# Kernel optimization log

Measured on AMD Instinct MI355X. Metric: run time of the kernel, lower is better.

Reference implementation:

```python
import jax, jax.numpy as jnp
import numpy as np

DIM = 512
HEADS = 8
WINDOW = 128


def setup_inputs() -> dict:
    key = jax.random.key(0)
    k1, k2, k3, k4 = jax.random.split(key, 4)
    x = jax.random.normal(k1, (16, 4096, DIM), dtype=jnp.float32)
    w_qkv = jax.random.normal(k2, (3 * DIM, DIM), dtype=jnp.float32) * 0.02
    w_proj = jax.random.normal(k3, (DIM, DIM), dtype=jnp.float32) * 0.02
    b_proj = jax.random.normal(k4, (DIM,), dtype=jnp.float32) * 0.02
    return {"x": x, "w_qkv": w_qkv, "w_proj": w_proj, "b_proj": b_proj}


def reference(x, w_qkv, w_proj, b_proj):
    B0, T0, C = x.shape
    H = HEADS
    hd = C // H
    scale = hd ** (-0.5)
    W = WINDOW
    # split into independent windows: [B*T/W, W, C]
    xw = x.reshape(-1, W, C)
    Bw = xw.shape[0]
    # qkv projection (no bias), reshape to [3, Bw, H, W, hd]
    qkv = (xw @ w_qkv.T).reshape(Bw, W, 3, H, hd).transpose(2, 0, 3, 1, 4)
    q, k, v = qkv[0], qkv[1], qkv[2]
    # scaled scores per window: [Bw, H, W, W]
    attn = jnp.einsum("bhqd,bhkd->bhqk", q, k) * scale
    causal_mask = jnp.tril(jnp.ones((W, W), dtype=bool))
    attn = jnp.where(causal_mask, attn, -jnp.inf)
    attn = jax.nn.softmax(attn, axis=-1)
    out = jnp.einsum("bhqk,bhkd->bhqd", attn, v)  # [Bw, H, W, hd]
    out = out.transpose(0, 2, 1, 3).reshape(Bw, W, C)
    out = out @ w_proj.T + b_proj
    return out.reshape(B0, T0, C)
```

## Files before the change

### kernel.cpp

```cpp
#include <hip/hip_runtime.h>
#include <stdint.h>


typedef unsigned short ushort_t;
typedef __attribute__((ext_vector_type(8))) short short8;
typedef __attribute__((ext_vector_type(4))) float f32x4;
typedef __attribute__((ext_vector_type(4))) float f4v;
typedef __attribute__((ext_vector_type(4))) unsigned short us4;

static __device__ __forceinline__ unsigned short f2bf(float f) {
  unsigned int u = __float_as_uint(f);
  u += 0x7FFFu + ((u >> 16) & 1u);
  return (unsigned short)(u >> 16);
}

static __device__ __forceinline__ void gl_lds16(const ushort_t* g, ushort_t* l) {
  __builtin_amdgcn_global_load_lds(
      (const __attribute__((address_space(1))) void*)g,
      (__attribute__((address_space(3))) void*)l, 16, 0, 0);
}

__global__ __launch_bounds__(256) void cast_f32_bf16(const float* __restrict__ in,
                                                     ushort_t* __restrict__ out, int n4) {
  int i = blockIdx.x * 256 + threadIdx.x;
  if (i >= n4) return;
  f4v v = ((const f4v*)in)[i];
  us4 o;
  o.x = f2bf(v.x); o.y = f2bf(v.y); o.z = f2bf(v.z); o.w = f2bf(v.w);
  ((us4*)out)[i] = o;
}

__global__ __launch_bounds__(256) void qkv_gemm(const ushort_t* __restrict__ A,
                                                const ushort_t* __restrict__ B,
                                                ushort_t* __restrict__ qk,
                                                ushort_t* __restrict__ vT) {
  __shared__ __align__(16) ushort_t As[128 * 64];
  __shared__ __align__(16) ushort_t Bs[128 * 64];
  const int tid = threadIdx.x;
  const int lane = tid & 63;
  const int wv = tid >> 6;
  const int wr = wv >> 1, wc = wv & 1;
  const int m0 = blockIdx.y << 7;
  const int n0 = blockIdx.x << 7;
  const int lr = lane & 15;
  const int lg = lane >> 4;
  const int lk = lg << 3;

  f32x4 acc[4][4] = {};

  const int grow = tid >> 3;
  const int gcol = (tid & 7) << 3;
  const ushort_t* gA = A + (size_t)(m0 + grow) * 512 + gcol;
  const ushort_t* gB = B + (size_t)(n0 + grow) * 512 + gcol;

  for (int kk = 0; kk < 512; kk += 64) {
#pragma unroll
    for (int r = 0; r < 4; ++r) {
      gl_lds16(gA + (size_t)(r * 32) * 512 + kk, As + (size_t)(r * 256 + wv * 64) * 8);
      gl_lds16(gB + (size_t)(r * 32) * 512 + kk, Bs + (size_t)(r * 256 + wv * 64) * 8);
    }
    __syncthreads();
#pragma unroll
    for (int ks = 0; ks < 2; ++ks) {
      const int kb = ks * 32 + lk;
      short8 a[4], b[4];
#pragma unroll
      for (int mi = 0; mi < 4; ++mi)
        a[mi] = *(const short8*)(As + (wr * 64 + mi * 16 + lr) * 64 + kb);
#pragma unroll
      for (int ni = 0; ni < 4; ++ni)
        b[ni] = *(const short8*)(Bs + (wc * 64 + ni * 16 + lr) * 64 + kb);
#pragma unroll
      for (int mi = 0; mi < 4; ++mi)
#pragma unroll
        for (int ni = 0; ni < 4; ++ni)
          acc[mi][ni] = __builtin_amdgcn_mfma_f32_16x16x32_bf16(a[mi], b[ni], acc[mi][ni], 0, 0, 0);
    }
    __syncthreads();
  }

  if (n0 < 1024) {
#pragma unroll
    for (int mi = 0; mi < 4; ++mi) {
      const int rbase = m0 + wr * 64 + mi * 16 + lg * 4;
#pragma unroll
      for (int ni = 0; ni < 4; ++ni) {
        const int col = n0 + wc * 64 + ni * 16 + lr;
#pragma unroll
        for (int rg = 0; rg < 4; ++rg)
          qk[(size_t)(rbase + rg) * 1024 + col] = f2bf(acc[mi][ni][rg]);
      }
    }
  } else {
    const int win = blockIdx.y;
#pragma unroll
    for (int mi = 0; mi < 4; ++mi) {
      const int t0 = wr * 64 + mi * 16 + lg * 4;
#pragma unroll
      for (int ni = 0; ni < 4; ++ni) {
        const int c = n0 - 1024 + wc * 64 + ni * 16 + lr;
        const int h = c >> 6, d = c & 63;
        us4 o;
        o.x = f2bf(acc[mi][ni][0]); o.y = f2bf(acc[mi][ni][1]);
        o.z = f2bf(acc[mi][ni][2]); o.w = f2bf(acc[mi][ni][3]);
        *(us4*)(vT + (size_t)((win * 8 + h) * 64 + d) * 128 + t0) = o;
      }
    }
  }
}

__global__ __launch_bounds__(256) void attn_kernel(const ushort_t* __restrict__ qk,
                                                   const ushort_t* __restrict__ vT,
                                                   ushort_t* __restrict__ attn_out) {
  __shared__ __align__(16) ushort_t smem[27136];
  ushort_t* qs = smem;
  ushort_t* ks_ = smem + 9216;
  ushort_t* ps = smem;
  ushort_t* vs = smem + 18432;

  const int tid = threadIdx.x;
  const int lane = tid & 63;
  const int wv = tid >> 6;
  const int win = blockIdx.x >> 3;
  const int h = blockIdx.x & 7;
  const int lr = lane & 15;
  const int lg = lane >> 4;
  const int lk = lg << 3;

  const size_t qbase = (size_t)win * 128 * 1024 + h * 64;
#pragma unroll
  for (int r = 0; r < 4; ++r) {
    const int c = r * 256 + tid;
    const int t = c >> 3, d8 = (c & 7) << 3;
    short8 vq = *(const short8*)(qk + qbase + (size_t)t * 1024 + d8);
    short8 vk = *(const short8*)(qk + qbase + 512 + (size_t)t * 1024 + d8);
    *(short8*)(qs + t * 72 + d8) = vq;
    *(short8*)(ks_ + t * 72 + d8) = vk;
  }
  const size_t vbase = (size_t)(win * 8 + h) * 64 * 128;
#pragma unroll
  for (int r = 0; r < 4; ++r) {
    const int c = r * 256 + tid;
    const int d = c >> 4, t8 = (c & 15) << 3;
    short8 vvv = *(const short8*)(vT + vbase + (size_t)d * 128 + t8);
    *(short8*)(vs + d * 136 + t8) = vvv;
  }
  __syncthreads();

  const int r0 = wv * 32;
  const int ncol = 2 * (wv + 1);
  f32x4 sacc[2][8] = {};
#pragma unroll
  for (int ks2 = 0; ks2 < 2; ++ks2) {
    const int kb = ks2 * 32 + lk;
    short8 a0 = *(const short8*)(qs + (r0 + lr) * 72 + kb);
    short8 a1 = *(const short8*)(qs + (r0 + 16 + lr) * 72 + kb);
#pragma unroll
    for (int ni = 0; ni < 8; ++ni) {
      if (ni < ncol) {
        short8 b = *(const short8*)(ks_ + (ni * 16 + lr) * 72 + kb);
        sacc[0][ni] = __builtin_amdgcn_mfma_f32_16x16x32_bf16(a0, b, sacc[0][ni], 0, 0, 0);
        sacc[1][ni] = __builtin_amdgcn_mfma_f32_16x16x32_bf16(a1, b, sacc[1][ni], 0, 0, 0);
      }
    }
  }

  const float scale = 0.125f;
  float rs[2][4];
#pragma unroll
  for (int mi = 0; mi < 2; ++mi) {
#pragma unroll
    for (int rg = 0; rg < 4; ++rg) {
      const int row = r0 + mi * 16 + lg * 4 + rg;
      float m = -1e30f;
#pragma unroll
      for (int ni = 0; ni < 8; ++ni) {
        if (ni < ncol) {
          const int col = ni * 16 + lr;
          float v = sacc[mi][ni][rg] * scale;
          v = (col <= row) ? v : -1e30f;
          sacc[mi][ni][rg] = v;
          m = fmaxf(m, v);
        }
      }
      m = fmaxf(m, __shfl_xor(m, 1));
      m = fmaxf(m, __shfl_xor(m, 2));
      m = fmaxf(m, __shfl_xor(m, 4));
      m = fmaxf(m, __shfl_xor(m, 8));
      float s = 0.f;
#pragma unroll
      for (int ni = 0; ni < 8; ++ni) {
        if (ni < ncol) {
          float p = __expf(sacc[mi][ni][rg] - m);
          sacc[mi][ni][rg] = p;
          s += p;
        }
      }
      s += __shfl_xor(s, 1);
      s += __shfl_xor(s, 2);
      s += __shfl_xor(s, 4);
      s += __shfl_xor(s, 8);
      rs[mi][rg] = 1.0f / s;
    }
  }

  __syncthreads();

#pragma unroll
  for (int mi = 0; mi < 2; ++mi)
#pragma unroll
    for (int ni = 0; ni < 8; ++ni) {
      if (ni < ncol) {
#pragma unroll
        for (int rg = 0; rg < 4; ++rg) {
          const int row = r0 + mi * 16 + lg * 4 + rg;
          const int col = ni * 16 + lr;
          ps[row * 136 + col] = f2bf(sacc[mi][ni][rg]);
        }
      }
    }

  f32x4 oacc[2][4] = {};
#pragma unroll
  for (int ks2 = 0; ks2 < 4; ++ks2) {
    if (ks2 <= wv) {
      const int kb = ks2 * 32 + lk;
      short8 a0 = *(const short8*)(ps + (r0 + lr) * 136 + kb);
      short8 a1 = *(const short8*)(ps + (r0 + 16 + lr) * 136 + kb);
#pragma unroll
      for (int nd = 0; nd < 4; ++nd) {
        short8 b = *(const short8*)(vs + (nd * 16 + lr) * 136 + kb);
        oacc[0][nd] = __builtin_amdgcn_mfma_f32_16x16x32_bf16(a0, b, oacc[0][nd], 0, 0, 0);
        oacc[1][nd] = __builtin_amdgcn_mfma_f32_16x16x32_bf16(a1, b, oacc[1][nd], 0, 0, 0);
      }
    }
  }

  const size_t obase = (size_t)win * 128 * 512 + h * 64;
#pragma unroll
  for (int mi = 0; mi < 2; ++mi)
#pragma unroll
    for (int nd = 0; nd < 4; ++nd)
#pragma unroll
      for (int rg = 0; rg < 4; ++rg) {
        const int row = r0 + mi * 16 + lg * 4 + rg;
        const int col = nd * 16 + lr;
        attn_out[obase + (size_t)row * 512 + col] = f2bf(oacc[mi][nd][rg] * rs[mi][rg]);
      }
}

__global__ __launch_bounds__(256) void proj_gemm(const ushort_t* __restrict__ A,
                                                 const ushort_t* __restrict__ B,
                                                 const float* __restrict__ bias,
                                                 float* __restrict__ out) {
  __shared__ __align__(16) ushort_t As[128 * 64];
  __shared__ __align__(16) ushort_t Bs[128 * 64];
  const int tid = threadIdx.x;
  const int lane = tid & 63;
  const int wv = tid >> 6;
  const int wr = wv >> 1, wc = wv & 1;
  const int m0 = blockIdx.y << 7;
  const int n0 = blockIdx.x << 7;
  const int lr = lane & 15;
  const int lg = lane >> 4;
  const int lk = lg << 3;

  f32x4 acc[4][4] = {};

  const int grow = tid >> 3;
  const int gcol = (tid & 7) << 3;
  const ushort_t* gA = A + (size_t)(m0 + grow) * 512 + gcol;
  const ushort_t* gB = B + (size_t)(n0 + grow) * 512 + gcol;

  for (int kk = 0; kk < 512; kk += 64) {
#pragma unroll
    for (int r = 0; r < 4; ++r) {
      gl_lds16(gA + (size_t)(r * 32) * 512 + kk, As + (size_t)(r * 256 + wv * 64) * 8);
      gl_lds16(gB + (size_t)(r * 32) * 512 + kk, Bs + (size_t)(r * 256 + wv * 64) * 8);
    }
    __syncthreads();
#pragma unroll
    for (int ks = 0; ks < 2; ++ks) {
      const int kb = ks * 32 + lk;
      short8 a[4], b[4];
#pragma unroll
      for (int mi = 0; mi < 4; ++mi)
        a[mi] = *(const short8*)(As + (wr * 64 + mi * 16 + lr) * 64 + kb);
#pragma unroll
      for (int ni = 0; ni < 4; ++ni)
        b[ni] = *(const short8*)(Bs + (wc * 64 + ni * 16 + lr) * 64 + kb);
#pragma unroll
      for (int mi = 0; mi < 4; ++mi)
#pragma unroll
        for (int ni = 0; ni < 4; ++ni)
          acc[mi][ni] = __builtin_amdgcn_mfma_f32_16x16x32_bf16(a[mi], b[ni], acc[mi][ni], 0, 0, 0);
    }
    __syncthreads();
  }

#pragma unroll
  for (int mi = 0; mi < 4; ++mi) {
    const int rbase = m0 + wr * 64 + mi * 16 + lg * 4;
#pragma unroll
    for (int ni = 0; ni < 4; ++ni) {
      const int col = n0 + wc * 64 + ni * 16 + lr;
      const float bv = bias[col];
#pragma unroll
      for (int rg = 0; rg < 4; ++rg)
        out[(size_t)(rbase + rg) * 512 + col] = acc[mi][ni][rg] + bv;
    }
  }
}

extern "C" void kernel_launch(void* const* d_in, const int* in_sizes, int n_in,
                              void* d_out, int out_size, void* d_ws, size_t ws_size,
                              hipStream_t stream) {
  const float* x      = (const float*)d_in[0];
  const float* w_qkv  = (const float*)d_in[1];
  const float* w_proj = (const float*)d_in[2];
  const float* b_proj = (const float*)d_in[3];
  float* out = (float*)d_out;

  char* ws = (char*)d_ws;
  ushort_t* x_bf     = (ushort_t*)(ws);
  ushort_t* qk_ws    = (ushort_t*)(ws + 67108864);
  ushort_t* vT_ws    = (ushort_t*)(ws + 67108864 + 134217728);
  ushort_t* attn_ws  = (ushort_t*)(ws + 67108864 + 134217728 + 67108864);
  ushort_t* wqkv_bf  = (ushort_t*)(ws + 335544320);
  ushort_t* wproj_bf = (ushort_t*)(ws + 337117184);

  cast_f32_bf16<<<32768, 256, 0, stream>>>(x, x_bf, 8388608);
  cast_f32_bf16<<<768, 256, 0, stream>>>(w_qkv, wqkv_bf, 196608);
  cast_f32_bf16<<<256, 256, 0, stream>>>(w_proj, wproj_bf, 65536);

  qkv_gemm<<<dim3(12, 512), 256, 0, stream>>>(x_bf, wqkv_bf, qk_ws, vT_ws);
  attn_kernel<<<4096, 256, 0, stream>>>(qk_ws, vT_ws, attn_ws);
  proj_gemm<<<dim3(4, 512), 256, 0, stream>>>(attn_ws, wproj_bf, b_proj, out);
}
```

Before: 547.7 us.

## Swizzle GEMM LDS tiles and balance causal attention work across waves

```diff
diff --git a/kernel.cpp b/kernel.cpp
--- a/kernel.cpp
+++ b/kernel.cpp
@@ -44,12 +44,12 @@
   const int n0 = blockIdx.x << 7;
   const int lr = lane & 15;
   const int lg = lane >> 4;
-  const int lk = lg << 3;
+  const int sw = lr & 7;
 
   f32x4 acc[4][4] = {};
 
   const int grow = tid >> 3;
-  const int gcol = (tid & 7) << 3;
+  const int gcol = (((tid & 7) ^ (grow & 7)) << 3);
   const ushort_t* gA = A + (size_t)(m0 + grow) * 512 + gcol;
   const ushort_t* gB = B + (size_t)(n0 + grow) * 512 + gcol;
 
@@ -62,14 +62,14 @@
     __syncthreads();
 #pragma unroll
     for (int ks = 0; ks < 2; ++ks) {
-      const int kb = ks * 32 + lk;
+      const int co = ((((ks << 2) | lg) ^ sw) << 3);
       short8 a[4], b[4];
 #pragma unroll
       for (int mi = 0; mi < 4; ++mi)
-        a[mi] = *(const short8*)(As + (wr * 64 + mi * 16 + lr) * 64 + kb);
+        a[mi] = *(const short8*)(As + (wr * 64 + mi * 16 + lr) * 64 + co);
 #pragma unroll
       for (int ni = 0; ni < 4; ++ni)
-        b[ni] = *(const short8*)(Bs + (wc * 64 + ni * 16 + lr) * 64 + kb);
+        b[ni] = *(const short8*)(Bs + (wc * 64 + ni * 16 + lr) * 64 + co);
 #pragma unroll
       for (int mi = 0; mi < 4; ++mi)
 #pragma unroll
@@ -79,10 +79,11 @@
     __syncthreads();
   }
 
+  const int lg4 = lg << 2;
   if (n0 < 1024) {
 #pragma unroll
     for (int mi = 0; mi < 4; ++mi) {
-      const int rbase = m0 + wr * 64 + mi * 16 + lg * 4;
+      const int rbase = m0 + wr * 64 + mi * 16 + lg4;
 #pragma unroll
       for (int ni = 0; ni < 4; ++ni) {
         const int col = n0 + wc * 64 + ni * 16 + lr;
@@ -95,7 +96,7 @@
     const int win = blockIdx.y;
 #pragma unroll
     for (int mi = 0; mi < 4; ++mi) {
-      const int t0 = wr * 64 + mi * 16 + lg * 4;
+      const int t0 = wr * 64 + mi * 16 + lg4;
 #pragma unroll
       for (int ni = 0; ni < 4; ++ni) {
         const int c = n0 - 1024 + wc * 64 + ni * 16 + lr;
@@ -112,11 +113,11 @@
 __global__ __launch_bounds__(256) void attn_kernel(const ushort_t* __restrict__ qk,
                                                    const ushort_t* __restrict__ vT,
                                                    ushort_t* __restrict__ attn_out) {
-  __shared__ __align__(16) ushort_t smem[27136];
+  __shared__ __align__(16) ushort_t smem[25856];
   ushort_t* qs = smem;
-  ushort_t* ks_ = smem + 9216;
+  ushort_t* ks_ = smem + 8704;
+  ushort_t* vs = smem + 17408;
   ushort_t* ps = smem;
-  ushort_t* vs = smem + 18432;
 
   const int tid = threadIdx.x;
   const int lane = tid & 63;
@@ -126,6 +127,7 @@
   const int lr = lane & 15;
   const int lg = lane >> 4;
   const int lk = lg << 3;
+  const int lg4 = lg << 2;
 
   const size_t qbase = (size_t)win * 128 * 1024 + h * 64;
 #pragma unroll
@@ -134,8 +136,8 @@
     const int t = c >> 3, d8 = (c & 7) << 3;
     short8 vq = *(const short8*)(qk + qbase + (size_t)t * 1024 + d8);
     short8 vk = *(const short8*)(qk + qbase + 512 + (size_t)t * 1024 + d8);
-    *(short8*)(qs + t * 72 + d8) = vq;
-    *(short8*)(ks_ + t * 72 + d8) = vk;
+    *(short8*)(qs + t * 68 + d8) = vq;
+    *(short8*)(ks_ + t * 68 + d8) = vk;
   }
   const size_t vbase = (size_t)(win * 8 + h) * 64 * 128;
 #pragma unroll
@@ -143,23 +145,24 @@
     const int c = r * 256 + tid;
     const int d = c >> 4, t8 = (c & 15) << 3;
     short8 vvv = *(const short8*)(vT + vbase + (size_t)d * 128 + t8);
-    *(short8*)(vs + d * 136 + t8) = vvv;
+    *(short8*)(vs + d * 132 + t8) = vvv;
   }
   __syncthreads();
 
-  const int r0 = wv * 32;
-  const int ncol = 2 * (wv + 1);
+  const int rt[2] = {wv, 7 - wv};
+
   f32x4 sacc[2][8] = {};
 #pragma unroll
   for (int ks2 = 0; ks2 < 2; ++ks2) {
     const int kb = ks2 * 32 + lk;
-    short8 a0 = *(const short8*)(qs + (r0 + lr) * 72 + kb);
-    short8 a1 = *(const short8*)(qs + (r0 + 16 + lr) * 72 + kb);
+    short8 a0 = *(const short8*)(qs + (rt[0] * 16 + lr) * 68 + kb);
+    short8 a1 = *(const short8*)(qs + (rt[1] * 16 + lr) * 68 + kb);
 #pragma unroll
     for (int ni = 0; ni < 8; ++ni) {
-      if (ni < ncol) {
-        short8 b = *(const short8*)(ks_ + (ni * 16 + lr) * 72 + kb);
-        sacc[0][ni] = __builtin_amdgcn_mfma_f32_16x16x32_bf16(a0, b, sacc[0][ni], 0, 0, 0);
+      if (ni <= rt[1]) {
+        short8 b = *(const short8*)(ks_ + (ni * 16 + lr) * 68 + kb);
+        if (ni <= rt[0])
+          sacc[0][ni] = __builtin_amdgcn_mfma_f32_16x16x32_bf16(a0, b, sacc[0][ni], 0, 0, 0);
         sacc[1][ni] = __builtin_amdgcn_mfma_f32_16x16x32_bf16(a1, b, sacc[1][ni], 0, 0, 0);
       }
     }
@@ -169,13 +172,14 @@
   float rs[2][4];
 #pragma unroll
   for (int mi = 0; mi < 2; ++mi) {
+    const int rb = rt[mi] * 16;
 #pragma unroll
     for (int rg = 0; rg < 4; ++rg) {
-      const int row = r0 + mi * 16 + lg * 4 + rg;
+      const int row = rb + lg4 + rg;
       float m = -1e30f;
 #pragma unroll
       for (int ni = 0; ni < 8; ++ni) {
-        if (ni < ncol) {
+        if (ni <= rt[mi]) {
           const int col = ni * 16 + lr;
           float v = sacc[mi][ni][rg] * scale;
           v = (col <= row) ? v : -1e30f;
@@ -190,7 +194,7 @@
       float s = 0.f;
 #pragma unroll
       for (int ni = 0; ni < 8; ++ni) {
-        if (ni < ncol) {
+        if (ni <= rt[mi]) {
           float p = __expf(sacc[mi][ni][rg] - m);
           sacc[mi][ni][rg] = p;
           s += p;
@@ -207,46 +211,59 @@
   __syncthreads();
 
 #pragma unroll
-  for (int mi = 0; mi < 2; ++mi)
+  for (int mi = 0; mi < 2; ++mi) {
+    const int r = rt[mi];
+    const int rb = r * 16;
 #pragma unroll
     for (int ni = 0; ni < 8; ++ni) {
-      if (ni < ncol) {
-#pragma unroll
-        for (int rg = 0; rg < 4; ++rg) {
-          const int row = r0 + mi * 16 + lg * 4 + rg;
-          const int col = ni * 16 + lr;
-          ps[row * 136 + col] = f2bf(sacc[mi][ni][rg]);
+      if (ni <= r) {
+#pragma unroll
+        for (int rg = 0; rg < 4; ++rg)
+          ps[(rb + lg4 + rg) * 132 + ni * 16 + lr] = f2bf(sacc[mi][ni][rg]);
+      }
+    }
+    if (!(r & 1)) {
+#pragma unroll
+      for (int rg = 0; rg < 4; ++rg)
+        ps[(rb + lg4 + rg) * 132 + (r + 1) * 16 + lr] = 0;
+    }
+  }
+
+  f32x4 oacc[2][4] = {};
+#pragma unroll
+  for (int ks2 = 0; ks2 < 4; ++ks2) {
+    const int kb = ks2 * 32 + lk;
+    if (ks2 <= (rt[1] >> 1)) {
+      short8 a1 = *(const short8*)(ps + (rt[1] * 16 + lr) * 132 + kb);
+#pragma unroll
+      for (int nd = 0; nd < 4; ++nd) {
+        short8 b = *(const short8*)(vs + (nd * 16 + lr) * 132 + kb);
+        oacc[1][nd] = __builtin_amdgcn_mfma_f32_16x16x32_bf16(a1, b, oacc[1][nd], 0, 0, 0);
+      }
+      if (ks2 <= (rt[0] >> 1)) {
+        short8 a0 = *(const short8*)(ps + (rt[0] * 16 + lr) * 132 + kb);
+#pragma unroll
+        for (int nd = 0; nd < 4; ++nd) {
+          short8 b = *(const short8*)(vs + (nd * 16 + lr) * 132 + kb);
+          oacc[0][nd] = __builtin_amdgcn_mfma_f32_16x16x32_bf16(a0, b, oacc[0][nd], 0, 0, 0);
         }
       }
     }
-
-  f32x4 oacc[2][4] = {};
-#pragma unroll
-  for (int ks2 = 0; ks2 < 4; ++ks2) {
-    if (ks2 <= wv) {
-      const int kb = ks2 * 32 + lk;
-      short8 a0 = *(const short8*)(ps + (r0 + lr) * 136 + kb);
-      short8 a1 = *(const short8*)(ps + (r0 + 16 + lr) * 136 + kb);
-#pragma unroll
-      for (int nd = 0; nd < 4; ++nd) {
-        short8 b = *(const short8*)(vs + (nd * 16 + lr) * 136 + kb);
-        oacc[0][nd] = __builtin_amdgcn_mfma_f32_16x16x32_bf16(a0, b, oacc[0][nd], 0, 0, 0);
-        oacc[1][nd] = __builtin_amdgcn_mfma_f32_16x16x32_bf16(a1, b, oacc[1][nd], 0, 0, 0);
-      }
-    }
   }
 
   const size_t obase = (size_t)win * 128 * 512 + h * 64;
 #pragma unroll
-  for (int mi = 0; mi < 2; ++mi)
+  for (int mi = 0; mi < 2; ++mi) {
+    const int rb = rt[mi] * 16;
 #pragma unroll
     for (int nd = 0; nd < 4; ++nd)
 #pragma unroll
       for (int rg = 0; rg < 4; ++rg) {
-        const int row = r0 + mi * 16 + lg * 4 + rg;
+        const int row = rb + lg4 + rg;
         const int col = nd * 16 + lr;
         attn_out[obase + (size_t)row * 512 + col] = f2bf(oacc[mi][nd][rg] * rs[mi][rg]);
       }
+  }
 }
 
 __global__ __launch_bounds__(256) void proj_gemm(const ushort_t* __restrict__ A,
@@ -263,12 +280,12 @@
   const int n0 = blockIdx.x << 7;
   const int lr = lane & 15;
   const int lg = lane >> 4;
-  const int lk = lg << 3;
+  const int sw = lr & 7;
 
   f32x4 acc[4][4] = {};
 
   const int grow = tid >> 3;
-  const int gcol = (tid & 7) << 3;
+  const int gcol = (((tid & 7) ^ (grow & 7)) << 3);
   const ushort_t* gA = A + (size_t)(m0 + grow) * 512 + gcol;
   const ushort_t* gB = B + (size_t)(n0 + grow) * 512 + gcol;
 
@@ -281,14 +298,14 @@
     __syncthreads();
 #pragma unroll
     for (int ks = 0; ks < 2; ++ks) {
-      const int kb = ks * 32 + lk;
+      const int co = ((((ks << 2) | lg) ^ sw) << 3);
       short8 a[4], b[4];
 #pragma unroll
       for (int mi = 0; mi < 4; ++mi)
-        a[mi] = *(const short8*)(As + (wr * 64 + mi * 16 + lr) * 64 + kb);
+        a[mi] = *(const short8*)(As + (wr * 64 + mi * 16 + lr) * 64 + co);
 #pragma unroll
       for (int ni = 0; ni < 4; ++ni)
-        b[ni] = *(const short8*)(Bs + (wc * 64 + ni * 16 + lr) * 64 + kb);
+        b[ni] = *(const short8*)(Bs + (wc * 64 + ni * 16 + lr) * 64 + co);
 #pragma unroll
       for (int mi = 0; mi < 4; ++mi)
 #pragma unroll
@@ -298,9 +315,10 @@
     __syncthreads();
   }
 
+  const int lg4 = lg << 2;
 #pragma unroll
   for (int mi = 0; mi < 4; ++mi) {
-    const int rbase = m0 + wr * 64 + mi * 16 + lg * 4;
+    const int rbase = m0 + wr * 64 + mi * 16 + lg4;
 #pragma unroll
     for (int ni = 0; ni < 4; ++ni) {
       const int col = n0 + wc * 64 + ni * 16 + lr;
```

After: 550.9 us. No clear change (+0.6%).
